# Performance work log

Hardware: AMD Instinct MI355X
Metric: run time of the kernel (lower is better)

Reference implementation:

```python
import jax, jax.numpy as jnp
import numpy as np

HEADS = 20
SHIFT = 0.6931471805599453  # style_alignment_score_shift = log(2)
KEY_SCALE = 1.0             # style_alignment_score_scale
EPS = 1e-5


def expand_first(feat, scale=1.0):
    # feat: [B, H, S, D]; broadcast style features (batch items 0 and B//2)
    b = feat.shape[0]
    fs = jnp.stack([feat[0], feat[b // 2]])[:, None]           # [2,1,H,S,D]
    fs = jnp.broadcast_to(fs, (2, b // 2) + feat.shape[1:])    # [2,B/2,H,S,D]
    if scale != 1:
        fs = jnp.concatenate([fs[:, :1], scale * fs[:, 1:]], axis=1)
    return fs.reshape(feat.shape)


def concat_first(feat, scale=1.0):
    # concatenate style features along the sequence axis (-2)
    return jnp.concatenate([feat, expand_first(feat, scale=scale)], axis=-2)


def adain(feat):
    # stats over sequence axis (-2); torch .var() is unbiased (ddof=1)
    mean = feat.mean(axis=-2, keepdims=True)
    std = jnp.sqrt(feat.var(axis=-2, keepdims=True, ddof=1) + EPS)
    sm = expand_first(mean)
    ss = expand_first(std)
    return (feat - mean) / std * ss + sm


def setup_inputs() -> dict:
    key = jax.random.key(0)
    ks = jax.random.split(key, 6)
    B, S, C = 4, 1024, 1280
    sc = 1.0 / np.sqrt(C)
    return {
        "hidden_states": jax.random.normal(ks[0], (B, S, C), jnp.float32),
        "Wq": jax.random.normal(ks[1], (C, C), jnp.float32) * sc,
        "Wk": jax.random.normal(ks[2], (C, C), jnp.float32) * sc,
        "Wv": jax.random.normal(ks[3], (C, C), jnp.float32) * sc,
        "Wo": jax.random.normal(ks[4], (C, C), jnp.float32) * sc,
        "bo": jnp.zeros((C,), jnp.float32),
    }


def reference(hidden_states, Wq, Wk, Wv, Wo, bo):
    B, S, C = hidden_states.shape
    H = HEADS
    hd = C // H
    scale = hd ** -0.5

    def to_heads(t):  # [B,S,C] -> [B,H,S,hd]
        return t.reshape(B, S, H, hd).transpose(0, 2, 1, 3)

    q = to_heads(hidden_states @ Wq.T)
    k = to_heads(hidden_states @ Wk.T)
    v = to_heads(hidden_states @ Wv.T)

    q = adain(q)              # adain_queries
    k = adain(k)              # adain_keys
    # adain_values = False

    k = concat_first(k, scale=KEY_SCALE)   # [B,H,2S,hd]
    v = concat_first(v)                    # [B,H,2S,hd]

    # shifted scaled dot-product attention (shift added to shared-key block)
    logits = jnp.einsum('bhqd,bhkd->bhqk', q, k) * scale  # [B,H,S,2S]
    bias = jnp.where(jnp.arange(k.shape[-2]) >= S, jnp.float32(SHIFT), jnp.float32(0.0))
    probs = jax.nn.softmax(logits + bias, axis=-1)
    out = jnp.einsum('bhqk,bhkd->bhqd', probs, v)         # [B,H,S,hd]

    out = out.transpose(0, 2, 1, 3).reshape(B, S, C)
    out = out @ Wo.T + bo
    return out
```

## Files before the change

### kernel.cpp

```cpp
#include <hip/hip_runtime.h>
#include <math.h>


typedef __bf16 bf16x8 __attribute__((ext_vector_type(8)));
typedef float f32x4 __attribute__((ext_vector_type(4)));
typedef unsigned short u16x8 __attribute__((ext_vector_type(8)));

#define BDIM 256

__device__ inline unsigned short f2bf(float f) {
  unsigned int u = __float_as_uint(f);
  u += 0x7fffu + ((u >> 16) & 1u);
  return (unsigned short)(u >> 16);
}
__device__ inline unsigned int pack_bf2(float lo, float hi) {
  return (unsigned int)f2bf(lo) | ((unsigned int)f2bf(hi) << 16);
}
__device__ inline float bf2f(unsigned short h) {
  return __uint_as_float(((unsigned int)h) << 16);
}

__device__ inline void gl_lds16(const unsigned short* g, unsigned short* l) {
  __builtin_amdgcn_global_load_lds(
      (const __attribute__((address_space(1))) unsigned int*)g,
      (__attribute__((address_space(3))) unsigned int*)l, 16, 0, 0);
}

__global__ __launch_bounds__(BDIM) void k_convert_all(
    const float* __restrict__ X, const float* __restrict__ Wq,
    const float* __restrict__ Wk, const float* __restrict__ Wv,
    const float* __restrict__ Wo, unsigned short* __restrict__ Xbf,
    unsigned short* __restrict__ Wcat, unsigned short* __restrict__ Wobf) {
  const int idx = blockIdx.x * BDIM + threadIdx.x;
  const float* src;
  unsigned short* dst;
  int off;
  if (idx < 1310720) {
    src = X; dst = Xbf; off = idx;
  } else {
    const int r = idx - 1310720;
    const int which = r / 409600;
    off = r - which * 409600;
    src = (which == 0) ? Wq : (which == 1) ? Wk : (which == 2) ? Wv : Wo;
    dst = (which < 3) ? Wcat + (size_t)which * 1638400 : Wobf;
  }
  const float4 v = ((const float4*)src)[off];
  ushort4 o;
  o.x = f2bf(v.x); o.y = f2bf(v.y); o.z = f2bf(v.z); o.w = f2bf(v.w);
  ((ushort4*)dst)[off] = o;
}

__global__ __launch_bounds__(BDIM) void k_gemm_bf16(
    const unsigned short* __restrict__ A, const unsigned short* __restrict__ B,
    unsigned short* __restrict__ Cbf, int M, int N, int K) {
  __shared__ unsigned short As[128 * 32];
  __shared__ unsigned short Bs[128 * 32];
  const int t = threadIdx.x;
  const int w = t >> 6, lane = t & 63, quad = lane >> 4, l16 = lane & 15;
  const int wm = (w >> 1) << 6, wn = (w & 1) << 6;
  const int mBase = blockIdx.x * 128, nBase = blockIdx.y * 128;

  f32x4 acc[4][4];
#pragma unroll
  for (int i = 0; i < 4; i++)
#pragma unroll
    for (int j = 0; j < 4; j++) acc[i][j] = (f32x4){0.f, 0.f, 0.f, 0.f};

  const int r0 = t >> 2;
  const int kk0 = (t & 3) * 8;

  for (int k0 = 0; k0 < K; k0 += 32) {
    gl_lds16(A + (size_t)(mBase + r0) * K + k0 + kk0, As + t * 8);
    gl_lds16(A + (size_t)(mBase + 64 + r0) * K + k0 + kk0, As + (t + 256) * 8);
    gl_lds16(B + (size_t)(nBase + r0) * K + k0 + kk0, Bs + t * 8);
    gl_lds16(B + (size_t)(nBase + 64 + r0) * K + k0 + kk0, Bs + (t + 256) * 8);
    __syncthreads();
    bf16x8 af[4], bfr[4];
#pragma unroll
    for (int i = 0; i < 4; i++)
      af[i] = *(const bf16x8*)(As + (wm + i * 16 + l16) * 32 + quad * 8);
#pragma unroll
    for (int i = 0; i < 4; i++)
      bfr[i] = *(const bf16x8*)(Bs + (wn + i * 16 + l16) * 32 + quad * 8);
#pragma unroll
    for (int mi = 0; mi < 4; mi++)
#pragma unroll
      for (int ni = 0; ni < 4; ni++)
        acc[mi][ni] = __builtin_amdgcn_mfma_f32_16x16x32_bf16(
            af[mi], bfr[ni], acc[mi][ni], 0, 0, 0);
    __syncthreads();
  }

#pragma unroll
  for (int mi = 0; mi < 4; mi++)
#pragma unroll
    for (int r = 0; r < 4; r++) {
      const int row = mBase + wm + mi * 16 + quad * 4 + r;
#pragma unroll
      for (int ni = 0; ni < 4; ni++)
        Cbf[(size_t)row * N + nBase + wn + ni * 16 + l16] = f2bf(acc[mi][ni][r]);
    }
}

__global__ __launch_bounds__(BDIM) void k_gemm_64x128(
    const unsigned short* __restrict__ A, const unsigned short* __restrict__ B,
    float* __restrict__ Cf, const float* __restrict__ bias, int M, int N,
    int K) {
  __shared__ unsigned short As[64 * 32];
  __shared__ unsigned short Bs[128 * 32];
  const int t = threadIdx.x;
  const int w = t >> 6, lane = t & 63, quad = lane >> 4, l16 = lane & 15;
  const int wm = (w >> 1) << 5, wn = (w & 1) << 6;
  const int mBase = blockIdx.x * 64, nBase = blockIdx.y * 128;

  f32x4 acc[2][4];
#pragma unroll
  for (int i = 0; i < 2; i++)
#pragma unroll
    for (int j = 0; j < 4; j++) acc[i][j] = (f32x4){0.f, 0.f, 0.f, 0.f};

  const int r0 = t >> 2;
  const int kk0 = (t & 3) * 8;

  for (int k0 = 0; k0 < K; k0 += 32) {
    gl_lds16(A + (size_t)(mBase + r0) * K + k0 + kk0, As + t * 8);
    gl_lds16(B + (size_t)(nBase + r0) * K + k0 + kk0, Bs + t * 8);
    gl_lds16(B + (size_t)(nBase + 64 + r0) * K + k0 + kk0, Bs + (t + 256) * 8);
    __syncthreads();
    bf16x8 af[2], bfr[4];
#pragma unroll
    for (int i = 0; i < 2; i++)
      af[i] = *(const bf16x8*)(As + (wm + i * 16 + l16) * 32 + quad * 8);
#pragma unroll
    for (int i = 0; i < 4; i++)
      bfr[i] = *(const bf16x8*)(Bs + (wn + i * 16 + l16) * 32 + quad * 8);
#pragma unroll
    for (int mi = 0; mi < 2; mi++)
#pragma unroll
      for (int ni = 0; ni < 4; ni++)
        acc[mi][ni] = __builtin_amdgcn_mfma_f32_16x16x32_bf16(
            af[mi], bfr[ni], acc[mi][ni], 0, 0, 0);
    __syncthreads();
  }

#pragma unroll
  for (int mi = 0; mi < 2; mi++)
#pragma unroll
    for (int r = 0; r < 4; r++) {
      const int row = mBase + wm + mi * 16 + quad * 4 + r;
#pragma unroll
      for (int ni = 0; ni < 4; ni++) {
        const int col = nBase + wn + ni * 16 + l16;
        Cf[(size_t)row * N + col] = acc[mi][ni][r] + bias[col];
      }
    }
}

__global__ __launch_bounds__(320) void k_stats1(
    const unsigned short* __restrict__ QKV, float* __restrict__ psum,
    float* __restrict__ psq) {
  const int z = blockIdx.y, which = z >> 2, b = z & 3;
  const int c = threadIdx.x * 4;
  const size_t base =
      (size_t)(b * 1024 + blockIdx.x * 32) * 3840 + which * 1280 + c;
  float4 s = {0.f, 0.f, 0.f, 0.f}, s2 = {0.f, 0.f, 0.f, 0.f};
#pragma unroll 8
  for (int i = 0; i < 32; ++i) {
    const ushort4 xv = *(const ushort4*)(QKV + base + (size_t)i * 3840);
    const float x0 = bf2f(xv.x), x1 = bf2f(xv.y), x2 = bf2f(xv.z),
                x3 = bf2f(xv.w);
    s.x += x0; s.y += x1; s.z += x2; s.w += x3;
    s2.x = fmaf(x0, x0, s2.x); s2.y = fmaf(x1, x1, s2.y);
    s2.z = fmaf(x2, x2, s2.z); s2.w = fmaf(x3, x3, s2.w);
  }
  const size_t o = ((size_t)z * 32 + blockIdx.x) * 1280 + c;
  *(float4*)(psum + o) = s;
  *(float4*)(psq + o) = s2;
}

__global__ __launch_bounds__(BDIM) void k_stats2(
    const float* __restrict__ psum, const float* __restrict__ psq,
    float* __restrict__ stats) {
  const int z = blockIdx.y, which = z >> 2, b = z & 3;
  const int c = blockIdx.x * 256 + threadIdx.x;
  float s = 0.f, s2 = 0.f;
#pragma unroll
  for (int j = 0; j < 32; ++j) {
    s += psum[((size_t)z * 32 + j) * 1280 + c];
    s2 += psq[((size_t)z * 32 + j) * 1280 + c];
  }
  const float mean = s * (1.0f / 1024.0f);
  const float var = (s2 - 1024.0f * mean * mean) * (1.0f / 1023.0f);
  stats[((which * 2 + 0) * 4 + b) * 1280 + c] = mean;
  stats[((which * 2 + 1) * 4 + b) * 1280 + c] = sqrtf(var + 1e-5f);
}

__global__ __launch_bounds__(BDIM) void k_adain(
    const unsigned short* __restrict__ QKV, const float* __restrict__ stats,
    unsigned short* __restrict__ qn, unsigned short* __restrict__ kn) {
  const int which = blockIdx.z, b = blockIdx.y;
  const int idx = blockIdx.x * BDIM + threadIdx.x;
  const int s = idx / 320;
  const int c = (idx - s * 320) * 4;
  const int sb = (b < 2) ? 0 : 2;
  const ushort4 xv =
      *(const ushort4*)(QKV + ((size_t)(b * 1024 + s)) * 3840 + which * 1280 + c);
  const float4 mean = *(const float4*)(stats + ((which * 2 + 0) * 4 + b) * 1280 + c);
  const float4 stdv = *(const float4*)(stats + ((which * 2 + 1) * 4 + b) * 1280 + c);
  const float4 meanS = *(const float4*)(stats + ((which * 2 + 0) * 4 + sb) * 1280 + c);
  const float4 stdS = *(const float4*)(stats + ((which * 2 + 1) * 4 + sb) * 1280 + c);
  ushort4 o;
  o.x = f2bf((bf2f(xv.x) - mean.x) / stdv.x * stdS.x + meanS.x);
  o.y = f2bf((bf2f(xv.y) - mean.y) / stdv.y * stdS.y + meanS.y);
  o.z = f2bf((bf2f(xv.z) - mean.z) / stdv.z * stdS.z + meanS.z);
  o.w = f2bf((bf2f(xv.w) - mean.w) / stdv.w * stdS.w + meanS.w);
  unsigned short* dst = (which == 0) ? qn : kn;
  *(ushort4*)(dst + ((size_t)(b * 1024 + s)) * 1280 + c) = o;
}

__global__ __launch_bounds__(BDIM) void k_transpose_v(
    const unsigned short* __restrict__ QKV, unsigned short* __restrict__ vt) {
  __shared__ unsigned short tile[64][65];
  const int s0 = blockIdx.x * 64, c0 = blockIdx.y * 64, b = blockIdx.z;
  const int t = threadIdx.x;
  const int r = t >> 2, seg = (t & 3) * 16;
  const size_t goff = ((size_t)(b * 1024 + s0 + r)) * 3840 + 2560 + c0 + seg;
  const u16x8 va = *(const u16x8*)(QKV + goff);
  const u16x8 vb = *(const u16x8*)(QKV + goff + 8);
#pragma unroll
  for (int j = 0; j < 8; j++) {
    tile[r][seg + j] = va[j];
    tile[r][seg + 8 + j] = vb[j];
  }
  __syncthreads();
  u16x8 o0, o1;
#pragma unroll
  for (int j = 0; j < 8; j++) {
    o0[j] = tile[seg + j][r];
    o1[j] = tile[seg + 8 + j][r];
  }
  const size_t ooff = ((size_t)(b * 1280 + c0 + r)) * 1024 + s0 + seg;
  *(u16x8*)(vt + ooff) = o0;
  *(u16x8*)(vt + ooff + 8) = o1;
}

__global__ __launch_bounds__(BDIM, 4) void k_attn(
    const unsigned short* __restrict__ qn, const unsigned short* __restrict__ kn,
    const unsigned short* __restrict__ vt, unsigned short* __restrict__ Opart,
    float* __restrict__ Lpart) {
  const int S = 1024, C = 1280;
  const int qt = blockIdx.x, h = blockIdx.y, zs = blockIdx.z;
  int b, chunk;
  if (zs < 2)      { b = 0; chunk = zs; }
  else if (zs < 6) { b = 1; chunk = zs - 2; }
  else if (zs < 8) { b = 2; chunk = zs - 6; }
  else             { b = 3; chunk = zs - 8; }
  const int ktBeg = chunk * 8;
  const int t = threadIdx.x, w = t >> 6, lane = t & 63;
  const int quad = lane >> 4, l16 = lane & 15;
  const int bstyle = (b < 2) ? 0 : 2;
  const int qrow = qt * 128 + w * 32;

  __shared__ unsigned short Ks[2][2][64 * 32];
  __shared__ unsigned short Vs[2][64 * 32];
  __shared__ unsigned short Plds[4][32][64];

  bf16x8 aq[2][2];
#pragma unroll
  for (int g = 0; g < 2; ++g) {
    const size_t qoff =
        ((size_t)(b * S + qrow + g * 16 + l16)) * C + h * 64 + quad * 8;
    aq[g][0] = *(const bf16x8*)(qn + qoff);
    aq[g][1] = *(const bf16x8*)(qn + qoff + 32);
  }

  bf16x8 ones;
#pragma unroll
  for (int i = 0; i < 8; ++i) ones[i] = (__bf16)1.0f;

  f32x4 o[2][4], lsum[2];
#pragma unroll
  for (int g = 0; g < 2; ++g) {
    lsum[g] = (f32x4){0.f, 0.f, 0.f, 0.f};
#pragma unroll
    for (int i = 0; i < 4; i++) o[g][i] = (f32x4){0.f, 0.f, 0.f, 0.f};
  }

  const int krow = t >> 2;
  const int kseg = (t & 3) * 8;
  const int sw = l16 & 14;

  auto stageK = [&](int buf, int kt) {
    const int bs = (kt < 16) ? b : bstyle;
    const int sk = (kt & 15) * 64;
    const unsigned short* kg =
        kn + (size_t)(bs * S + sk + krow) * C + h * 64 + kseg;
    gl_lds16(kg, Ks[buf][0] + t * 8);
    gl_lds16(kg + 32, Ks[buf][1] + t * 8);
  };
  auto stageV = [&](int kt) {
    const int bs = (kt < 16) ? b : bstyle;
    const int sk = (kt & 15) * 64;
    const unsigned short* vg =
        vt + (size_t)(bs * C + h * 64 + krow) * S + sk + kseg;
    gl_lds16(vg, Vs[0] + t * 8);
    gl_lds16(vg + 32, Vs[1] + t * 8);
  };

  stageK(0, ktBeg);

  const float SCALE2 = 0.125f * 1.44269504088896341f;

  for (int i = 0; i < 8; ++i) {
    const int kt = ktBeg + i;
    const int buf = i & 1;
    __syncthreads();
    stageV(kt);
    if (i + 1 < 8) stageK(buf ^ 1, kt + 1);

    const float bias2 = (kt >= 16) ? 1.0f : 0.0f;

    f32x4 z2[2][4];
#pragma unroll
    for (int nt = 0; nt < 4; ++nt) {
      const bf16x8 bk0 =
          *(const bf16x8*)(Ks[buf][0] + (nt * 16 + l16) * 32 + quad * 8);
      const bf16x8 bk1 =
          *(const bf16x8*)(Ks[buf][1] + (nt * 16 + l16) * 32 + quad * 8);
#pragma unroll
      for (int g = 0; g < 2; ++g) {
        f32x4 zz = (f32x4){0.f, 0.f, 0.f, 0.f};
        zz = __builtin_amdgcn_mfma_f32_16x16x32_bf16(bk0, aq[g][0], zz, 0, 0, 0);
        zz = __builtin_amdgcn_mfma_f32_16x16x32_bf16(bk1, aq[g][1], zz, 0, 0, 0);
        z2[g][nt] = zz;
      }
    }

#pragma unroll
    for (int g = 0; g < 2; ++g) {
#pragma unroll
      for (int nt = 0; nt < 4; ++nt) {
        const float e0 = exp2f(fmaf(z2[g][nt][0], SCALE2, bias2));
        const float e1 = exp2f(fmaf(z2[g][nt][1], SCALE2, bias2));
        const float e2 = exp2f(fmaf(z2[g][nt][2], SCALE2, bias2));
        const float e3 = exp2f(fmaf(z2[g][nt][3], SCALE2, bias2));
        uint2 pk;
        pk.x = pack_bf2(e0, e1);
        pk.y = pack_bf2(e2, e3);
        const int phys = (nt * 4 + quad) ^ sw;
        *(uint2*)(&Plds[w][g * 16 + l16][phys * 4]) = pk;
      }
    }

    __syncthreads();

#pragma unroll
    for (int g = 0; g < 2; ++g) {
      const int a0 = (2 * quad) ^ sw;
      const int a1 = (2 * quad + 8) ^ sw;
      const bf16x8 pa0 = *(const bf16x8*)(&Plds[w][g * 16 + l16][a0 * 4]);
      const bf16x8 pa1 = *(const bf16x8*)(&Plds[w][g * 16 + l16][a1 * 4]);
      lsum[g] = __builtin_amdgcn_mfma_f32_16x16x32_bf16(pa0, ones, lsum[g], 0, 0, 0);
      lsum[g] = __builtin_amdgcn_mfma_f32_16x16x32_bf16(pa1, ones, lsum[g], 0, 0, 0);
#pragma unroll
      for (int dt = 0; dt < 4; ++dt) {
        const bf16x8 vb0 =
            *(const bf16x8*)(Vs[0] + (dt * 16 + l16) * 32 + quad * 8);
        const bf16x8 vb1 =
            *(const bf16x8*)(Vs[1] + (dt * 16 + l16) * 32 + quad * 8);
        o[g][dt] =
            __builtin_amdgcn_mfma_f32_16x16x32_bf16(pa0, vb0, o[g][dt], 0, 0, 0);
        o[g][dt] =
            __builtin_amdgcn_mfma_f32_16x16x32_bf16(pa1, vb1, o[g][dt], 0, 0, 0);
      }
    }
  }

  if (l16 == 0) {
#pragma unroll
    for (int g = 0; g < 2; ++g)
#pragma unroll
      for (int r = 0; r < 4; ++r)
        Lpart[((size_t)zs * 20 + h) * 1024 + qrow + g * 16 + quad * 4 + r] =
            lsum[g][r];
  }

  unsigned short* Op = Opart + (size_t)zs * 1024 * 1280;
#pragma unroll
  for (int g = 0; g < 2; ++g)
#pragma unroll
    for (int dt = 0; dt < 4; ++dt)
#pragma unroll
      for (int r = 0; r < 4; ++r)
        Op[(size_t)(qrow + g * 16 + quad * 4 + r) * 1280 + h * 64 + dt * 16 +
           l16] = f2bf(o[g][dt][r]);
}

__global__ __launch_bounds__(BDIM) void k_combine(
    const unsigned short* __restrict__ Opart, const float* __restrict__ Lpart,
    unsigned short* __restrict__ attnb) {
  const int idx = blockIdx.x * BDIM + threadIdx.x;
  const int row = idx / 160;
  const int c = (idx - row * 160) * 8;
  const int b = row >> 10, q = row & 1023, h = c >> 6;
  const int zb = (b >> 1) * 6 + (b & 1) * 2;
  const int ns = 2 + (b & 1) * 2;
  float L = 0.f;
  float acc[8] = {0.f, 0.f, 0.f, 0.f, 0.f, 0.f, 0.f, 0.f};
  for (int s = 0; s < ns; ++s) {
    L += Lpart[((size_t)(zb + s) * 20 + h) * 1024 + q];
    const u16x8 v =
        *(const u16x8*)(Opart + (size_t)(zb + s) * 1310720 + (size_t)q * 1280 + c);
#pragma unroll
    for (int j = 0; j < 8; ++j) acc[j] += bf2f(v[j]);
  }
  const float rl = 1.0f / L;
  u16x8 o8;
#pragma unroll
  for (int j = 0; j < 8; ++j) o8[j] = f2bf(acc[j] * rl);
  *(u16x8*)(attnb + (size_t)row * 1280 + c) = o8;
}

extern "C" void kernel_launch(void* const* d_in, const int* in_sizes, int n_in,
                              void* d_out, int out_size, void* d_ws,
                              size_t ws_size, hipStream_t stream) {
  const float* X = (const float*)d_in[0];
  const float* Wq = (const float*)d_in[1];
  const float* Wk = (const float*)d_in[2];
  const float* Wv = (const float*)d_in[3];
  const float* Wo = (const float*)d_in[4];
  const float* bo = (const float*)d_in[5];
  float* out = (float*)d_out;

  char* ws = (char*)d_ws;
  size_t off = 0;
  auto alloc = [&](size_t bytes) {
    char* p = ws + off;
    off += (bytes + 255) & ~(size_t)255;
    return p;
  };
  unsigned short* Wcat = (unsigned short*)alloc(3840ull * 1280 * 2);
  unsigned short* Xbf = (unsigned short*)alloc(4096ull * 1280 * 2);
  unsigned short* QKV = (unsigned short*)alloc(4096ull * 3840 * 2);
  unsigned short* Wobf = (unsigned short*)alloc(1280ull * 1280 * 2);
  float* stats = (float*)alloc(2ull * 2 * 4 * 1280 * 4);
  unsigned short* qnb = (unsigned short*)alloc(4096ull * 1280 * 2);
  unsigned short* knb = (unsigned short*)alloc(4096ull * 1280 * 2);
  unsigned short* vtb = (unsigned short*)alloc(4096ull * 1280 * 2);
  unsigned short* attnb = (unsigned short*)alloc(4096ull * 1280 * 2);

  unsigned short* Opart = QKV;
  float* Lpart = (float*)Wcat;
  float* psum = (float*)attnb;
  float* psq = (float*)(attnb + 4096ull * 1280 / 2);

  k_convert_all<<<11520, BDIM, 0, stream>>>(X, Wq, Wk, Wv, Wo, Xbf, Wcat, Wobf);
  k_gemm_bf16<<<dim3(32, 30), BDIM, 0, stream>>>(Xbf, Wcat, QKV, 4096, 3840,
                                                 1280);
  k_stats1<<<dim3(32, 8), 320, 0, stream>>>(QKV, psum, psq);
  k_stats2<<<dim3(5, 8), BDIM, 0, stream>>>(psum, psq, stats);
  k_adain<<<dim3(1280, 4, 2), BDIM, 0, stream>>>(QKV, stats, qnb, knb);
  k_transpose_v<<<dim3(16, 20, 4), BDIM, 0, stream>>>(QKV, vtb);
  k_attn<<<dim3(8, 20, 12), BDIM, 0, stream>>>(qnb, knb, vtb, Opart, Lpart);
  k_combine<<<2560, BDIM, 0, stream>>>(Opart, Lpart, attnb);
  k_gemm_64x128<<<dim3(64, 10), BDIM, 0, stream>>>(attnb, Wobf, out, bo, 4096,
                                                   1280, 1280);
}
```

Measured before the change: 297.4 us.

## Double-buffer attention V, deepen GEMM K-steps, fuse adain with V transpose

Both GEMM kernels now load two 32-wide K slices per iteration and run twice as many MFMAs between barriers, so barrier and issue overhead per unit of work drops, at the cost of more LDS. The adain and V-transpose kernels are merged into one launch over a flat grid, removing one kernel launch. In attention, V gets its own double buffer staged together with K one tile ahead. The separate V stage and the barrier before the P·V step are removed; that barrier is not needed because each wave uses only its own Plds slice. The occupancy hint is lowered from 4 to 3 to cover the larger shared memory footprint.

```diff
diff --git a/kernel.cpp b/kernel.cpp
--- a/kernel.cpp
+++ b/kernel.cpp
@@ -53,8 +53,8 @@
 __global__ __launch_bounds__(BDIM) void k_gemm_bf16(
     const unsigned short* __restrict__ A, const unsigned short* __restrict__ B,
     unsigned short* __restrict__ Cbf, int M, int N, int K) {
-  __shared__ unsigned short As[128 * 32];
-  __shared__ unsigned short Bs[128 * 32];
+  __shared__ unsigned short As[2][128 * 32];
+  __shared__ unsigned short Bs[2][128 * 32];
   const int t = threadIdx.x;
   const int w = t >> 6, lane = t & 63, quad = lane >> 4, l16 = lane & 15;
   const int wm = (w >> 1) << 6, wn = (w & 1) << 6;
@@ -69,25 +69,34 @@
   const int r0 = t >> 2;
   const int kk0 = (t & 3) * 8;
 
-  for (int k0 = 0; k0 < K; k0 += 32) {
-    gl_lds16(A + (size_t)(mBase + r0) * K + k0 + kk0, As + t * 8);
-    gl_lds16(A + (size_t)(mBase + 64 + r0) * K + k0 + kk0, As + (t + 256) * 8);
-    gl_lds16(B + (size_t)(nBase + r0) * K + k0 + kk0, Bs + t * 8);
-    gl_lds16(B + (size_t)(nBase + 64 + r0) * K + k0 + kk0, Bs + (t + 256) * 8);
-    __syncthreads();
-    bf16x8 af[4], bfr[4];
-#pragma unroll
-    for (int i = 0; i < 4; i++)
-      af[i] = *(const bf16x8*)(As + (wm + i * 16 + l16) * 32 + quad * 8);
-#pragma unroll
-    for (int i = 0; i < 4; i++)
-      bfr[i] = *(const bf16x8*)(Bs + (wn + i * 16 + l16) * 32 + quad * 8);
-#pragma unroll
-    for (int mi = 0; mi < 4; mi++)
-#pragma unroll
-      for (int ni = 0; ni < 4; ni++)
-        acc[mi][ni] = __builtin_amdgcn_mfma_f32_16x16x32_bf16(
-            af[mi], bfr[ni], acc[mi][ni], 0, 0, 0);
+  for (int k0 = 0; k0 < K; k0 += 64) {
+    const unsigned short* Ab = A + (size_t)(mBase + r0) * K + k0 + kk0;
+    const unsigned short* Bb = B + (size_t)(nBase + r0) * K + k0 + kk0;
+    gl_lds16(Ab, As[0] + t * 8);
+    gl_lds16(Ab + (size_t)64 * K, As[0] + (t + 256) * 8);
+    gl_lds16(Ab + 32, As[1] + t * 8);
+    gl_lds16(Ab + (size_t)64 * K + 32, As[1] + (t + 256) * 8);
+    gl_lds16(Bb, Bs[0] + t * 8);
+    gl_lds16(Bb + (size_t)64 * K, Bs[0] + (t + 256) * 8);
+    gl_lds16(Bb + 32, Bs[1] + t * 8);
+    gl_lds16(Bb + (size_t)64 * K + 32, Bs[1] + (t + 256) * 8);
+    __syncthreads();
+    bf16x8 af[2][4], bfr[2][4];
+#pragma unroll
+    for (int hh = 0; hh < 2; hh++)
+#pragma unroll
+      for (int i = 0; i < 4; i++) {
+        af[hh][i] = *(const bf16x8*)(As[hh] + (wm + i * 16 + l16) * 32 + quad * 8);
+        bfr[hh][i] = *(const bf16x8*)(Bs[hh] + (wn + i * 16 + l16) * 32 + quad * 8);
+      }
+#pragma unroll
+    for (int hh = 0; hh < 2; hh++)
+#pragma unroll
+      for (int mi = 0; mi < 4; mi++)
+#pragma unroll
+        for (int ni = 0; ni < 4; ni++)
+          acc[mi][ni] = __builtin_amdgcn_mfma_f32_16x16x32_bf16(
+              af[hh][mi], bfr[hh][ni], acc[mi][ni], 0, 0, 0);
     __syncthreads();
   }
 
@@ -106,8 +115,8 @@
     const unsigned short* __restrict__ A, const unsigned short* __restrict__ B,
     float* __restrict__ Cf, const float* __restrict__ bias, int M, int N,
     int K) {
-  __shared__ unsigned short As[64 * 32];
-  __shared__ unsigned short Bs[128 * 32];
+  __shared__ unsigned short As[2][64 * 32];
+  __shared__ unsigned short Bs[2][128 * 32];
   const int t = threadIdx.x;
   const int w = t >> 6, lane = t & 63, quad = lane >> 4, l16 = lane & 15;
   const int wm = (w >> 1) << 5, wn = (w & 1) << 6;
@@ -122,24 +131,34 @@
   const int r0 = t >> 2;
   const int kk0 = (t & 3) * 8;
 
-  for (int k0 = 0; k0 < K; k0 += 32) {
-    gl_lds16(A + (size_t)(mBase + r0) * K + k0 + kk0, As + t * 8);
-    gl_lds16(B + (size_t)(nBase + r0) * K + k0 + kk0, Bs + t * 8);
-    gl_lds16(B + (size_t)(nBase + 64 + r0) * K + k0 + kk0, Bs + (t + 256) * 8);
-    __syncthreads();
-    bf16x8 af[2], bfr[4];
-#pragma unroll
-    for (int i = 0; i < 2; i++)
-      af[i] = *(const bf16x8*)(As + (wm + i * 16 + l16) * 32 + quad * 8);
-#pragma unroll
-    for (int i = 0; i < 4; i++)
-      bfr[i] = *(const bf16x8*)(Bs + (wn + i * 16 + l16) * 32 + quad * 8);
-#pragma unroll
-    for (int mi = 0; mi < 2; mi++)
-#pragma unroll
-      for (int ni = 0; ni < 4; ni++)
-        acc[mi][ni] = __builtin_amdgcn_mfma_f32_16x16x32_bf16(
-            af[mi], bfr[ni], acc[mi][ni], 0, 0, 0);
+  for (int k0 = 0; k0 < K; k0 += 64) {
+    const unsigned short* Ab = A + (size_t)(mBase + r0) * K + k0 + kk0;
+    const unsigned short* Bb = B + (size_t)(nBase + r0) * K + k0 + kk0;
+    gl_lds16(Ab, As[0] + t * 8);
+    gl_lds16(Ab + 32, As[1] + t * 8);
+    gl_lds16(Bb, Bs[0] + t * 8);
+    gl_lds16(Bb + (size_t)64 * K, Bs[0] + (t + 256) * 8);
+    gl_lds16(Bb + 32, Bs[1] + t * 8);
+    gl_lds16(Bb + (size_t)64 * K + 32, Bs[1] + (t + 256) * 8);
+    __syncthreads();
+    bf16x8 af[2][2], bfr[2][4];
+#pragma unroll
+    for (int hh = 0; hh < 2; hh++) {
+#pragma unroll
+      for (int i = 0; i < 2; i++)
+        af[hh][i] = *(const bf16x8*)(As[hh] + (wm + i * 16 + l16) * 32 + quad * 8);
+#pragma unroll
+      for (int i = 0; i < 4; i++)
+        bfr[hh][i] = *(const bf16x8*)(Bs[hh] + (wn + i * 16 + l16) * 32 + quad * 8);
+    }
+#pragma unroll
+    for (int hh = 0; hh < 2; hh++)
+#pragma unroll
+      for (int mi = 0; mi < 2; mi++)
+#pragma unroll
+        for (int ni = 0; ni < 4; ni++)
+          acc[mi][ni] = __builtin_amdgcn_mfma_f32_16x16x32_bf16(
+              af[hh][mi], bfr[hh][ni], acc[mi][ni], 0, 0, 0);
     __syncthreads();
   }
 
@@ -195,56 +214,68 @@
   stats[((which * 2 + 1) * 4 + b) * 1280 + c] = sqrtf(var + 1e-5f);
 }
 
-__global__ __launch_bounds__(BDIM) void k_adain(
+__global__ __launch_bounds__(BDIM) void k_adain_vt(
     const unsigned short* __restrict__ QKV, const float* __restrict__ stats,
-    unsigned short* __restrict__ qn, unsigned short* __restrict__ kn) {
-  const int which = blockIdx.z, b = blockIdx.y;
-  const int idx = blockIdx.x * BDIM + threadIdx.x;
-  const int s = idx / 320;
-  const int c = (idx - s * 320) * 4;
-  const int sb = (b < 2) ? 0 : 2;
-  const ushort4 xv =
-      *(const ushort4*)(QKV + ((size_t)(b * 1024 + s)) * 3840 + which * 1280 + c);
-  const float4 mean = *(const float4*)(stats + ((which * 2 + 0) * 4 + b) * 1280 + c);
-  const float4 stdv = *(const float4*)(stats + ((which * 2 + 1) * 4 + b) * 1280 + c);
-  const float4 meanS = *(const float4*)(stats + ((which * 2 + 0) * 4 + sb) * 1280 + c);
-  const float4 stdS = *(const float4*)(stats + ((which * 2 + 1) * 4 + sb) * 1280 + c);
-  ushort4 o;
-  o.x = f2bf((bf2f(xv.x) - mean.x) / stdv.x * stdS.x + meanS.x);
-  o.y = f2bf((bf2f(xv.y) - mean.y) / stdv.y * stdS.y + meanS.y);
-  o.z = f2bf((bf2f(xv.z) - mean.z) / stdv.z * stdS.z + meanS.z);
-  o.w = f2bf((bf2f(xv.w) - mean.w) / stdv.w * stdS.w + meanS.w);
-  unsigned short* dst = (which == 0) ? qn : kn;
-  *(ushort4*)(dst + ((size_t)(b * 1024 + s)) * 1280 + c) = o;
-}
-
-__global__ __launch_bounds__(BDIM) void k_transpose_v(
-    const unsigned short* __restrict__ QKV, unsigned short* __restrict__ vt) {
+    unsigned short* __restrict__ qn, unsigned short* __restrict__ kn,
+    unsigned short* __restrict__ vt) {
   __shared__ unsigned short tile[64][65];
-  const int s0 = blockIdx.x * 64, c0 = blockIdx.y * 64, b = blockIdx.z;
-  const int t = threadIdx.x;
-  const int r = t >> 2, seg = (t & 3) * 16;
-  const size_t goff = ((size_t)(b * 1024 + s0 + r)) * 3840 + 2560 + c0 + seg;
-  const u16x8 va = *(const u16x8*)(QKV + goff);
-  const u16x8 vb = *(const u16x8*)(QKV + goff + 8);
-#pragma unroll
-  for (int j = 0; j < 8; j++) {
-    tile[r][seg + j] = va[j];
-    tile[r][seg + 8 + j] = vb[j];
-  }
-  __syncthreads();
-  u16x8 o0, o1;
-#pragma unroll
-  for (int j = 0; j < 8; j++) {
-    o0[j] = tile[seg + j][r];
-    o1[j] = tile[seg + 8 + j][r];
-  }
-  const size_t ooff = ((size_t)(b * 1280 + c0 + r)) * 1024 + s0 + seg;
-  *(u16x8*)(vt + ooff) = o0;
-  *(u16x8*)(vt + ooff + 8) = o1;
-}
-
-__global__ __launch_bounds__(BDIM, 4) void k_attn(
+  const int bx = blockIdx.x;
+  if (bx < 10240) {
+    const int which = bx / 5120;
+    const int rem = bx - which * 5120;
+    const int b = rem / 1280;
+    const int xb = rem - b * 1280;
+    const int idx = xb * BDIM + threadIdx.x;
+    const int s = idx / 320;
+    const int c = (idx - s * 320) * 4;
+    const int sb = (b < 2) ? 0 : 2;
+    const ushort4 xv = *(const ushort4*)(QKV + ((size_t)(b * 1024 + s)) * 3840 +
+                                         which * 1280 + c);
+    const float4 mean =
+        *(const float4*)(stats + ((which * 2 + 0) * 4 + b) * 1280 + c);
+    const float4 stdv =
+        *(const float4*)(stats + ((which * 2 + 1) * 4 + b) * 1280 + c);
+    const float4 meanS =
+        *(const float4*)(stats + ((which * 2 + 0) * 4 + sb) * 1280 + c);
+    const float4 stdS =
+        *(const float4*)(stats + ((which * 2 + 1) * 4 + sb) * 1280 + c);
+    ushort4 o;
+    o.x = f2bf((bf2f(xv.x) - mean.x) / stdv.x * stdS.x + meanS.x);
+    o.y = f2bf((bf2f(xv.y) - mean.y) / stdv.y * stdS.y + meanS.y);
+    o.z = f2bf((bf2f(xv.z) - mean.z) / stdv.z * stdS.z + meanS.z);
+    o.w = f2bf((bf2f(xv.w) - mean.w) / stdv.w * stdS.w + meanS.w);
+    unsigned short* dst = (which == 0) ? qn : kn;
+    *(ushort4*)(dst + ((size_t)(b * 1024 + s)) * 1280 + c) = o;
+  } else {
+    const int tb = bx - 10240;
+    const int b = tb / 320;
+    const int r2 = tb - b * 320;
+    const int c0 = (r2 / 16) * 64;
+    const int s0 = (r2 & 15) * 64;
+    const int t = threadIdx.x;
+    const int r = t >> 2, seg = (t & 3) * 16;
+    const size_t goff = ((size_t)(b * 1024 + s0 + r)) * 3840 + 2560 + c0 + seg;
+    const u16x8 va = *(const u16x8*)(QKV + goff);
+    const u16x8 vb = *(const u16x8*)(QKV + goff + 8);
+#pragma unroll
+    for (int j = 0; j < 8; j++) {
+      tile[r][seg + j] = va[j];
+      tile[r][seg + 8 + j] = vb[j];
+    }
+    __syncthreads();
+    u16x8 o0, o1;
+#pragma unroll
+    for (int j = 0; j < 8; j++) {
+      o0[j] = tile[seg + j][r];
+      o1[j] = tile[seg + 8 + j][r];
+    }
+    const size_t ooff = ((size_t)(b * 1280 + c0 + r)) * 1024 + s0 + seg;
+    *(u16x8*)(vt + ooff) = o0;
+    *(u16x8*)(vt + ooff + 8) = o1;
+  }
+}
+
+__global__ __launch_bounds__(BDIM, 3) void k_attn(
     const unsigned short* __restrict__ qn, const unsigned short* __restrict__ kn,
     const unsigned short* __restrict__ vt, unsigned short* __restrict__ Opart,
     float* __restrict__ Lpart) {
@@ -262,7 +293,7 @@
   const int qrow = qt * 128 + w * 32;
 
   __shared__ unsigned short Ks[2][2][64 * 32];
-  __shared__ unsigned short Vs[2][64 * 32];
+  __shared__ unsigned short Vs[2][2][64 * 32];
   __shared__ unsigned short Plds[4][32][64];
 
   bf16x8 aq[2][2];
@@ -290,24 +321,20 @@
   const int kseg = (t & 3) * 8;
   const int sw = l16 & 14;
 
-  auto stageK = [&](int buf, int kt) {
+  auto stage = [&](int buf, int kt) {
     const int bs = (kt < 16) ? b : bstyle;
     const int sk = (kt & 15) * 64;
     const unsigned short* kg =
         kn + (size_t)(bs * S + sk + krow) * C + h * 64 + kseg;
     gl_lds16(kg, Ks[buf][0] + t * 8);
     gl_lds16(kg + 32, Ks[buf][1] + t * 8);
-  };
-  auto stageV = [&](int kt) {
-    const int bs = (kt < 16) ? b : bstyle;
-    const int sk = (kt & 15) * 64;
     const unsigned short* vg =
         vt + (size_t)(bs * C + h * 64 + krow) * S + sk + kseg;
-    gl_lds16(vg, Vs[0] + t * 8);
-    gl_lds16(vg + 32, Vs[1] + t * 8);
+    gl_lds16(vg, Vs[buf][0] + t * 8);
+    gl_lds16(vg + 32, Vs[buf][1] + t * 8);
   };
 
-  stageK(0, ktBeg);
+  stage(0, ktBeg);
 
   const float SCALE2 = 0.125f * 1.44269504088896341f;
 
@@ -315,8 +342,7 @@
     const int kt = ktBeg + i;
     const int buf = i & 1;
     __syncthreads();
-    stageV(kt);
-    if (i + 1 < 8) stageK(buf ^ 1, kt + 1);
+    if (i + 1 < 8) stage(buf ^ 1, kt + 1);
 
     const float bias2 = (kt >= 16) ? 1.0f : 0.0f;
 
@@ -352,8 +378,6 @@
       }
     }
 
-    __syncthreads();
-
 #pragma unroll
     for (int g = 0; g < 2; ++g) {
       const int a0 = (2 * quad) ^ sw;
@@ -365,9 +389,9 @@
 #pragma unroll
       for (int dt = 0; dt < 4; ++dt) {
         const bf16x8 vb0 =
-            *(const bf16x8*)(Vs[0] + (dt * 16 + l16) * 32 + quad * 8);
+            *(const bf16x8*)(Vs[buf][0] + (dt * 16 + l16) * 32 + quad * 8);
         const bf16x8 vb1 =
-            *(const bf16x8*)(Vs[1] + (dt * 16 + l16) * 32 + quad * 8);
+            *(const bf16x8*)(Vs[buf][1] + (dt * 16 + l16) * 32 + quad * 8);
         o[g][dt] =
             __builtin_amdgcn_mfma_f32_16x16x32_bf16(pa0, vb0, o[g][dt], 0, 0, 0);
         o[g][dt] =
@@ -459,8 +483,7 @@
                                                  1280);
   k_stats1<<<dim3(32, 8), 320, 0, stream>>>(QKV, psum, psq);
   k_stats2<<<dim3(5, 8), BDIM, 0, stream>>>(psum, psq, stats);
-  k_adain<<<dim3(1280, 4, 2), BDIM, 0, stream>>>(QKV, stats, qnb, knb);
-  k_transpose_v<<<dim3(16, 20, 4), BDIM, 0, stream>>>(QKV, vtb);
+  k_adain_vt<<<11520, BDIM, 0, stream>>>(QKV, stats, qnb, knb, vtb);
   k_attn<<<dim3(8, 20, 12), BDIM, 0, stream>>>(qnb, knb, vtb, Opart, Lpart);
   k_combine<<<2560, BDIM, 0, stream>>>(Opart, Lpart, attnb);
   k_gemm_64x128<<<dim3(64, 10), BDIM, 0, stream>>>(attnb, Wobf, out, bo, 4096,
```

Result: faster. 288.6 us (-3.0%).
